# Kernel tuning notes

Measured on AMD Instinct MI355X. Metric: run time of the kernel, lower is better.

## Reference

```python
import jax, jax.numpy as jnp
import numpy as np

HEADS = 8
EPS = 1e-4

def pixel_norm(x):
    # faithful to source: mean over dim=1 (token axis for [B,T,C] tensors)
    return x / jnp.sqrt(jnp.mean(x * x, axis=1, keepdims=True) + EPS)

def setup_inputs() -> dict:
    key = jax.random.key(0)
    ks = jax.random.split(key, 6)
    B, T, C = 4, 2048, 512
    s = 1.0 / np.sqrt(C)
    return {
        "hidden_states": jax.random.normal(ks[0], (B, T, C), jnp.float32),
        "Wq": jax.random.normal(ks[1], (C, C), jnp.float32) * s,
        "Wk": jax.random.normal(ks[2], (C, C), jnp.float32) * s,
        "Wv": jax.random.normal(ks[3], (C, C), jnp.float32) * s,
        "Wo": jax.random.normal(ks[4], (C, C), jnp.float32) * s,
        "bo": jnp.zeros((C,), jnp.float32),
    }

def reference(hidden_states, Wq, Wk, Wv, Wo, bo):
    B, T, C = hidden_states.shape
    H = HEADS
    d = C // H
    scale = 1.0 / np.sqrt(d)  # attn.scale = head_dim**-0.5
    residual = hidden_states

    q = pixel_norm(hidden_states @ Wq)  # [B,T,C]
    k = pixel_norm(hidden_states @ Wk)
    v = pixel_norm(hidden_states @ Wv)

    # head_to_batch_dim: [B,T,C] -> [B,H,T,d]
    def split_heads(x):
        return x.reshape(B, T, H, d).transpose(0, 2, 1, 3)
    q, k, v = split_heads(q), split_heads(k), split_heads(v)

    scores = jnp.einsum("bhqd,bhkd->bhqk", q, k) * scale
    probs = jax.nn.softmax(scores, axis=-1)
    out = jnp.einsum("bhqk,bhkd->bhqd", probs, v)  # [B,H,T,d]

    # batch_to_head_dim: [B,H,T,d] -> [B,T,C]
    out = out.transpose(0, 2, 1, 3).reshape(B, T, C)
    out = out @ Wo + bo  # to_out[0]; to_out[1] is dropout (identity in eval)
    out = out + residual  # residual_connection
    return out  # rescale_output_factor = 1.0
```

## Files before the change

kernel.cpp:

```cpp
#include <hip/hip_runtime.h>

#define Tt 2048
#define Cc 512
#define Bb 4
#define BC (Bb * Cc)

typedef __attribute__((ext_vector_type(4))) float f32x4;
typedef __attribute__((ext_vector_type(8))) _Float16 f16x8;
typedef __attribute__((ext_vector_type(4))) _Float16 f16x4;
typedef __attribute__((ext_vector_type(2))) _Float16 f16x2;

__device__ static inline void gl16(const _Float16* g, _Float16* l)
{
    __builtin_amdgcn_global_load_lds(
        (const __attribute__((address_space(1))) void*)g,
        (__attribute__((address_space(3))) void*)l, 16, 0, 0);
}

__global__ __launch_bounds__(256) void prep(
    const float* __restrict__ Wq, const float* __restrict__ Wk,
    const float* __restrict__ Wv, const float* __restrict__ Wo,
    const float* __restrict__ HS, _Float16* __restrict__ Wt,
    _Float16* __restrict__ HSh, float* __restrict__ colsum)
{
    const int blk = blockIdx.x;
    const int tid = threadIdx.x;
    __shared__ float tile[64][65];

    if (blk < 2048) {
        const size_t i = ((size_t)blk * 256 + tid) * 8;
        float4 a = *(const float4*)&HS[i];
        float4 b = *(const float4*)&HS[i + 4];
        f16x8 o;
        o[0] = (_Float16)a.x; o[1] = (_Float16)a.y;
        o[2] = (_Float16)a.z; o[3] = (_Float16)a.w;
        o[4] = (_Float16)b.x; o[5] = (_Float16)b.y;
        o[6] = (_Float16)b.z; o[7] = (_Float16)b.w;
        *(f16x8*)&HSh[i] = o;
    } else if (blk < 2304) {
        const int lb = blk - 2048;
        const int z = lb >> 6, x = lb & 63;
        const float* W = (z == 0) ? Wq : (z == 1) ? Wk : (z == 2) ? Wv : Wo;
        const int k0 = (x >> 3) * 64, n0 = (x & 7) * 64;
#pragma unroll
        for (int i = 0; i < 4; ++i) {
            const int idx = i * 256 + tid;
            const int kr = idx >> 4, c4 = idx & 15;
            float4 v = *(const float4*)&W[(size_t)(k0 + kr) * Cc + n0 + c4 * 4];
            tile[kr][c4 * 4 + 0] = v.x; tile[kr][c4 * 4 + 1] = v.y;
            tile[kr][c4 * 4 + 2] = v.z; tile[kr][c4 * 4 + 3] = v.w;
        }
        __syncthreads();
#pragma unroll
        for (int i = 0; i < 4; ++i) {
            const int idx = i * 256 + tid;
            const int nr = idx >> 4, k4 = idx & 15;
            f16x4 o;
            o[0] = (_Float16)tile[k4 * 4 + 0][nr];
            o[1] = (_Float16)tile[k4 * 4 + 1][nr];
            o[2] = (_Float16)tile[k4 * 4 + 2][nr];
            o[3] = (_Float16)tile[k4 * 4 + 3][nr];
            *(f16x4*)&Wt[((size_t)(z * 512 + n0 + nr)) * Cc + k0 + k4 * 4] = o;
        }
    } else {
        const int i = (blk - 2304) * 2048 + tid * 8;
        *(f32x4*)&colsum[i]     = (f32x4){0.f, 0.f, 0.f, 0.f};
        *(f32x4*)&colsum[i + 4] = (f32x4){0.f, 0.f, 0.f, 0.f};
    }
}

__global__ __launch_bounds__(256, 3) void qkv_mfma(
    const _Float16* __restrict__ HSh, const _Float16* __restrict__ Wt,
    _Float16* __restrict__ Qf, _Float16* __restrict__ Kf,
    _Float16* __restrict__ Vf, float* __restrict__ colsum)
{
    const int mt = blockIdx.x;
    const int nt = blockIdx.y;
    const int z  = blockIdx.z;
    _Float16* Out = (z == 0) ? Qf : (z == 1) ? Kf : Vf;

    const int tid = threadIdx.x;
    const int wave = tid >> 6, lane = tid & 63;
    const int quad = lane >> 4, lm = lane & 15;
    const int wm = (wave & 1) * 64, wn = (wave >> 1) * 64;

    __shared__ _Float16 sA[128 * 32];
    __shared__ _Float16 sB[128 * 32];

    f32x4 acc[4][4];
#pragma unroll
    for (int mf = 0; mf < 4; ++mf)
#pragma unroll
        for (int nf = 0; nf < 4; ++nf) acc[mf][nf] = (f32x4){0.f, 0.f, 0.f, 0.f};

    const int lr = lane >> 2;
    const int lc = (lane & 3) * 8;
    const _Float16* gaA = HSh + (size_t)(mt * 128 + wave * 32 + lr) * Cc + lc;
    const _Float16* gaB = Wt + ((size_t)(z * 512 + nt * 128 + wave * 32 + lr)) * Cc + lc;
    _Float16* ldA = &sA[wave * 1024];
    _Float16* ldB = &sB[wave * 1024];

    for (int k0 = 0; k0 < Cc; k0 += 32) {
        __syncthreads();
        gl16(gaA + k0,            ldA);
        gl16(gaA + 16 * Cc + k0,  ldA + 512);
        gl16(gaB + k0,            ldB);
        gl16(gaB + 16 * Cc + k0,  ldB + 512);
        __syncthreads();

        f16x8 ah[4], bh[4];
#pragma unroll
        for (int mf = 0; mf < 4; ++mf)
            ah[mf] = *(const f16x8*)&sA[(wm + mf * 16 + lm) * 32 + quad * 8];
#pragma unroll
        for (int nf = 0; nf < 4; ++nf)
            bh[nf] = *(const f16x8*)&sB[(wn + nf * 16 + lm) * 32 + quad * 8];
#pragma unroll
        for (int mf = 0; mf < 4; ++mf)
#pragma unroll
            for (int nf = 0; nf < 4; ++nf)
                acc[mf][nf] = __builtin_amdgcn_mfma_f32_16x16x32_f16(ah[mf], bh[nf], acc[mf][nf], 0, 0, 0);
    }

    const int bidx = mt >> 4;
#pragma unroll
    for (int nf = 0; nf < 4; ++nf) {
        float cs = 0.f;
#pragma unroll
        for (int mf = 0; mf < 4; ++mf)
#pragma unroll
            for (int r = 0; r < 4; ++r) {
                const float v = acc[mf][nf][r];
                const size_t idx =
                    (size_t)(mt * 128 + wm + mf * 16 + quad * 4 + r) * Cc +
                    nt * 128 + wn + nf * 16 + lm;
                Out[idx] = (_Float16)v;
                cs += v * v;
            }
        cs += __shfl_xor(cs, 16, 64);
        cs += __shfl_xor(cs, 32, 64);
        if (lane < 16)
            atomicAdd(&colsum[(size_t)z * BC + bidx * Cc + nt * 128 + wn + nf * 16 + lane], cs);
    }
}

__global__ __launch_bounds__(256) void norm_vt(
    const _Float16* __restrict__ V, _Float16* __restrict__ VT,
    const float* __restrict__ colsum, float* __restrict__ inv)
{
    const int blk = blockIdx.x;
    const int tid = threadIdx.x;

    __shared__ _Float16 tile[64 * 72];

    if (blk >= 1024) {
        const int i = (blk - 1024) * 256 + tid;
        inv[i] = rsqrtf(colsum[i] * (1.0f / Tt) + 1e-4f);
        return;
    }

    const int b = blk >> 8, ct = (blk >> 5) & 7, tt = blk & 31;
    const int t0 = tt * 64, c0 = ct * 64;

#pragma unroll
    for (int i = 0; i < 2; ++i) {
        const int idx = i * 256 + tid;
        const int tr = idx >> 3, c8 = (idx & 7) * 8;
        *(f16x8*)&tile[tr * 72 + c8] =
            *(const f16x8*)&V[(size_t)(b * Tt + t0 + tr) * Cc + c0 + c8];
    }
    __syncthreads();
#pragma unroll
    for (int i = 0; i < 2; ++i) {
        const int idx = i * 256 + tid;
        const int cr = idx >> 3, u = idx & 7;
        const int C0 = ((u >> 2) & 1) * 32 + (u & 1) * 16 + ((u >> 1) & 1) * 4;
        f16x4 oa, ob;
#pragma unroll
        for (int j = 0; j < 4; ++j) oa[j] = tile[(u * 8 + j) * 72 + cr];
#pragma unroll
        for (int j = 0; j < 4; ++j) ob[j] = tile[(u * 8 + 4 + j) * 72 + cr];
        _Float16* dst = &VT[(size_t)(b * Cc + c0 + cr) * Tt + t0];
        *(f16x4*)&dst[C0]     = oa;
        *(f16x4*)&dst[C0 + 8] = ob;
    }
}

#define LSTR 72

__global__ __launch_bounds__(256, 2) void attn_mfma(
    const _Float16* __restrict__ Qf, const _Float16* __restrict__ Kf,
    const _Float16* __restrict__ VT, const float* __restrict__ inv,
    _Float16* __restrict__ AO)
{
    const int bid = blockIdx.x;
    const int qt = bid >> 5;
    const int bh = bid & 31;
    const int b = bh >> 3, h = bh & 7;
    const int tid = threadIdx.x;
    const int wave = tid >> 6, lane = tid & 63;
    const int quad = lane >> 4, lm = lane & 15;

    __shared__ _Float16 sK[2][64 * LSTR];
    __shared__ _Float16 sVT[2][2][64 * LSTR];

    f16x8 qb[2][2];
    {
        const float* iqp = inv + b * Cc + h * 64;
        const float* ikp = inv + BC + b * Cc + h * 64;
#pragma unroll
        for (int qf = 0; qf < 2; ++qf) {
            const int row = qt * 128 + wave * 32 + qf * 16 + lm;
#pragma unroll
            for (int ks = 0; ks < 2; ++ks) {
                const int d0 = ks * 32 + quad * 8;
                f16x8 qv = *(const f16x8*)&Qf[(size_t)(b * Tt + row) * Cc + h * 64 + d0];
#pragma unroll
                for (int j = 0; j < 8; ++j) {
                    const float f = (float)qv[j] * iqp[d0 + j] * ikp[d0 + j] * 0.18033688011f;
                    qb[qf][ks][j] = (_Float16)f;
                }
            }
        }
    }

    f32x4 o[4][2];
#pragma unroll
    for (int cf = 0; cf < 4; ++cf)
#pragma unroll
        for (int qf = 0; qf < 2; ++qf) o[cf][qf] = (f32x4){0.f, 0.f, 0.f, 0.f};
    f32x4 ol[2];
#pragma unroll
    for (int qf = 0; qf < 2; ++qf) ol[qf] = (f32x4){0.f, 0.f, 0.f, 0.f};
    f16x8 ones;
#pragma unroll
    for (int j = 0; j < 8; ++j) ones[j] = (_Float16)1.0f;

    f16x8 pb[2][2];
#pragma unroll
    for (int qf = 0; qf < 2; ++qf)
#pragma unroll
        for (int ks = 0; ks < 2; ++ks)
#pragma unroll
            for (int j = 0; j < 8; ++j) pb[qf][ks][j] = (_Float16)0.0f;

    const int sr0 = tid >> 3, sc0 = (tid & 7) * 8;
    const int sr1 = sr0 + 32;
    const _Float16* gK = Kf + (size_t)b * Tt * Cc + h * 64;
    const _Float16* gV = VT + ((size_t)b * Cc + h * 64) * Tt;

    f16x8 rka0, rka1, rva0, rva1;
    f16x8 rkb0, rkb1, rvb0, rvb1;
    {
        rka0 = *(const f16x8*)&gK[(size_t)sr0 * Cc + sc0];
        rka1 = *(const f16x8*)&gK[(size_t)sr1 * Cc + sc0];
        rva0 = *(const f16x8*)&gV[(size_t)sr0 * Tt + sc0];
        rva1 = *(const f16x8*)&gV[(size_t)sr1 * Tt + sc0];
        rkb0 = *(const f16x8*)&gK[(size_t)(64 + sr0) * Cc + sc0];
        rkb1 = *(const f16x8*)&gK[(size_t)(64 + sr1) * Cc + sc0];
        rvb0 = *(const f16x8*)&gV[(size_t)sr0 * Tt + 64 + sc0];
        rvb1 = *(const f16x8*)&gV[(size_t)sr1 * Tt + 64 + sc0];
    }

#pragma unroll 2
    for (int r = 0; r < 16; ++r) {
        const int g = r & 1;

        __syncthreads();
        *(f16x8*)&sK[0][sr0 * LSTR + sc0] = rka0;
        *(f16x8*)&sK[0][sr1 * LSTR + sc0] = rka1;
        *(f16x8*)&sVT[g][0][sr0 * LSTR + sc0] = rva0;
        *(f16x8*)&sVT[g][0][sr1 * LSTR + sc0] = rva1;
        *(f16x8*)&sK[1][sr0 * LSTR + sc0] = rkb0;
        *(f16x8*)&sK[1][sr1 * LSTR + sc0] = rkb1;
        *(f16x8*)&sVT[g][1][sr0 * LSTR + sc0] = rvb0;
        *(f16x8*)&sVT[g][1][sr1 * LSTR + sc0] = rvb1;
        __syncthreads();

        if (r < 15) {
            const int tn = (r + 1) * 128;
            rka0 = *(const f16x8*)&gK[(size_t)(tn + sr0) * Cc + sc0];
            rka1 = *(const f16x8*)&gK[(size_t)(tn + sr1) * Cc + sc0];
            rva0 = *(const f16x8*)&gV[(size_t)sr0 * Tt + tn + sc0];
            rva1 = *(const f16x8*)&gV[(size_t)sr1 * Tt + tn + sc0];
            rkb0 = *(const f16x8*)&gK[(size_t)(tn + 64 + sr0) * Cc + sc0];
            rkb1 = *(const f16x8*)&gK[(size_t)(tn + 64 + sr1) * Cc + sc0];
            rvb0 = *(const f16x8*)&gV[(size_t)sr0 * Tt + tn + 64 + sc0];
            rvb1 = *(const f16x8*)&gV[(size_t)sr1 * Tt + tn + 64 + sc0];
        }

#pragma unroll
        for (int half = 0; half < 2; ++half) {
            f32x4 st[4][2];
#pragma unroll
            for (int kf = 0; kf < 4; ++kf)
#pragma unroll
                for (int qf = 0; qf < 2; ++qf) st[kf][qf] = (f32x4){0.f, 0.f, 0.f, 0.f};
#pragma unroll
            for (int ks = 0; ks < 2; ++ks) {
                f16x8 ka[4];
#pragma unroll
                for (int kf = 0; kf < 4; ++kf)
                    ka[kf] = *(const f16x8*)&sK[half][(kf * 16 + lm) * LSTR + ks * 32 + quad * 8];
                __builtin_amdgcn_s_setprio(1);
#pragma unroll
                for (int kf = 0; kf < 4; ++kf)
#pragma unroll
                    for (int qf = 0; qf < 2; ++qf)
                        st[kf][qf] = __builtin_amdgcn_mfma_f32_16x16x32_f16(ka[kf], qb[qf][ks], st[kf][qf], 0, 0, 0);
                __builtin_amdgcn_s_setprio(0);
            }

            if (half == 1 || r > 0) {
                const _Float16* sVp = (half == 0) ? sVT[g ^ 1][1] : sVT[g][0];
#pragma unroll
                for (int ks = 0; ks < 2; ++ks) {
                    f16x8 va[4];
#pragma unroll
                    for (int cf = 0; cf < 4; ++cf)
                        va[cf] = *(const f16x8*)&sVp[(cf * 16 + lm) * LSTR + ks * 32 + quad * 8];
                    __builtin_amdgcn_s_setprio(1);
#pragma unroll
                    for (int cf = 0; cf < 4; ++cf)
#pragma unroll
                        for (int qf = 0; qf < 2; ++qf)
                            o[cf][qf] = __builtin_amdgcn_mfma_f32_16x16x32_f16(va[cf], pb[qf][ks], o[cf][qf], 0, 0, 0);
#pragma unroll
                    for (int qf = 0; qf < 2; ++qf)
                        ol[qf] = __builtin_amdgcn_mfma_f32_16x16x32_f16(ones, pb[qf][ks], ol[qf], 0, 0, 0);
                    __builtin_amdgcn_s_setprio(0);
                }
            }

#pragma unroll
            for (int ks = 0; ks < 2; ++ks)
#pragma unroll
                for (int qf = 0; qf < 2; ++qf) {
                    const f32x4 a = st[2 * ks][qf];
                    const f32x4 c = st[2 * ks + 1][qf];
                    const f16x2 l0 = __builtin_bit_cast(f16x2, __builtin_amdgcn_cvt_pkrtz(
                        __builtin_amdgcn_exp2f(a[0]), __builtin_amdgcn_exp2f(a[1])));
                    const f16x2 l1 = __builtin_bit_cast(f16x2, __builtin_amdgcn_cvt_pkrtz(
                        __builtin_amdgcn_exp2f(a[2]), __builtin_amdgcn_exp2f(a[3])));
                    const f16x2 h0 = __builtin_bit_cast(f16x2, __builtin_amdgcn_cvt_pkrtz(
                        __builtin_amdgcn_exp2f(c[0]), __builtin_amdgcn_exp2f(c[1])));
                    const f16x2 h1 = __builtin_bit_cast(f16x2, __builtin_amdgcn_cvt_pkrtz(
                        __builtin_amdgcn_exp2f(c[2]), __builtin_amdgcn_exp2f(c[3])));
                    f16x8 p;
                    p[0] = l0[0]; p[1] = l0[1]; p[2] = l1[0]; p[3] = l1[1];
                    p[4] = h0[0]; p[5] = h0[1]; p[6] = h1[0]; p[7] = h1[1];
                    pb[qf][ks] = p;
                }
        }
    }

    {
        const _Float16* sVp = sVT[1][1];
#pragma unroll
        for (int ks = 0; ks < 2; ++ks) {
            f16x8 va[4];
#pragma unroll
            for (int cf = 0; cf < 4; ++cf)
                va[cf] = *(const f16x8*)&sVp[(cf * 16 + lm) * LSTR + ks * 32 + quad * 8];
#pragma unroll
            for (int cf = 0; cf < 4; ++cf)
#pragma unroll
                for (int qf = 0; qf < 2; ++qf)
                    o[cf][qf] = __builtin_amdgcn_mfma_f32_16x16x32_f16(va[cf], pb[qf][ks], o[cf][qf], 0, 0, 0);
#pragma unroll
            for (int qf = 0; qf < 2; ++qf)
                ol[qf] = __builtin_amdgcn_mfma_f32_16x16x32_f16(ones, pb[qf][ks], ol[qf], 0, 0, 0);
        }
    }

    float il[2];
#pragma unroll
    for (int qf = 0; qf < 2; ++qf) il[qf] = 1.0f / ol[qf][0];
    const float* ivp = inv + 2 * BC + b * Cc + h * 64;
    float iv[4][4];
#pragma unroll
    for (int cf = 0; cf < 4; ++cf) {
        float4 t = *(const float4*)&ivp[cf * 16 + quad * 4];
        iv[cf][0] = t.x; iv[cf][1] = t.y; iv[cf][2] = t.z; iv[cf][3] = t.w;
    }
#pragma unroll
    for (int qf = 0; qf < 2; ++qf) {
        const size_t row = (size_t)(b * Tt + qt * 128 + wave * 32 + qf * 16 + lm);
#pragma unroll
        for (int cf = 0; cf < 4; ++cf) {
            f16x4 pk;
#pragma unroll
            for (int r = 0; r < 4; ++r)
                pk[r] = (_Float16)(o[cf][qf][r] * il[qf] * iv[cf][r]);
            *(f16x4*)&AO[row * Cc + h * 64 + cf * 16 + quad * 4] = pk;
        }
    }
}

__global__ __launch_bounds__(256, 2) void out_mfma(
    const _Float16* __restrict__ AO, const _Float16* __restrict__ Wt,
    const float* __restrict__ bo, const float* __restrict__ HS,
    float* __restrict__ Outp)
{
    const int mt = blockIdx.x;
    const int nt = blockIdx.y;
    const int tid = threadIdx.x;
    const int wave = tid >> 6, lane = tid & 63;
    const int quad = lane >> 4, lm = lane & 15;
    const int wm = (wave & 1) * 32, wn = (wave >> 1) * 64;

    __shared__ _Float16 sA[64 * 32];
    __shared__ _Float16 sB[128 * 32];

    f32x4 acc[2][4];
#pragma unroll
    for (int mf = 0; mf < 2; ++mf)
#pragma unroll
        for (int nf = 0; nf < 4; ++nf) acc[mf][nf] = (f32x4){0.f, 0.f, 0.f, 0.f};

    const int lr = lane >> 2;
    const int lc = (lane & 3) * 8;
    const _Float16* gaA = AO + (size_t)(mt * 64 + wave * 16 + lr) * Cc + lc;
    const _Float16* gaB = Wt + ((size_t)(3 * 512 + nt * 128 + wave * 32 + lr)) * Cc + lc;
    _Float16* ldA = &sA[wave * 512];
    _Float16* ldB = &sB[wave * 1024];

    for (int k0 = 0; k0 < Cc; k0 += 32) {
        __syncthreads();
        gl16(gaA + k0,           ldA);
        gl16(gaB + k0,           ldB);
        gl16(gaB + 16 * Cc + k0, ldB + 512);
        __syncthreads();

        f16x8 ah[2], bh[4];
#pragma unroll
        for (int mf = 0; mf < 2; ++mf)
            ah[mf] = *(const f16x8*)&sA[(wm + mf * 16 + lm) * 32 + quad * 8];
#pragma unroll
        for (int nf = 0; nf < 4; ++nf)
            bh[nf] = *(const f16x8*)&sB[(wn + nf * 16 + lm) * 32 + quad * 8];
#pragma unroll
        for (int mf = 0; mf < 2; ++mf)
#pragma unroll
            for (int nf = 0; nf < 4; ++nf)
                acc[mf][nf] = __builtin_amdgcn_mfma_f32_16x16x32_f16(ah[mf], bh[nf], acc[mf][nf], 0, 0, 0);
    }

#pragma unroll
    for (int mf = 0; mf < 2; ++mf)
#pragma unroll
        for (int r = 0; r < 4; ++r) {
            const size_t m = (size_t)(mt * 64 + wm + mf * 16 + quad * 4 + r);
#pragma unroll
            for (int nf = 0; nf < 4; ++nf) {
                const int col = nt * 128 + wn + nf * 16 + lm;
                Outp[m * Cc + col] = acc[mf][nf][r] + bo[col] + HS[m * Cc + col];
            }
        }
}

extern "C" void kernel_launch(void* const* d_in, const int* in_sizes, int n_in,
                              void* d_out, int out_size, void* d_ws,
                              size_t ws_size, hipStream_t stream)
{
    const float* HS = (const float*)d_in[0];
    const float* Wq = (const float*)d_in[1];
    const float* Wk = (const float*)d_in[2];
    const float* Wv = (const float*)d_in[3];
    const float* Wo = (const float*)d_in[4];
    const float* bo = (const float*)d_in[5];
    float* out = (float*)d_out;

    const size_t SZ = (size_t)Bb * Tt * Cc;
    _Float16* Qf  = (_Float16*)d_ws;
    _Float16* Kf  = Qf + SZ;
    _Float16* Vf  = Kf + SZ;
    _Float16* VTh = Vf + SZ;
    _Float16* AO  = VTh + SZ;
    _Float16* Wt  = AO + SZ;
    float* colsum = (float*)(Wt + 4 * Cc * Cc);
    float* inv    = colsum + 3 * BC;

    _Float16* HSh = VTh;

    prep<<<2307, 256, 0, stream>>>(Wq, Wk, Wv, Wo, HS, Wt, HSh, colsum);

    qkv_mfma<<<dim3(64, 4, 3), 256, 0, stream>>>(HSh, Wt, Qf, Kf, Vf, colsum);

    norm_vt<<<1048, 256, 0, stream>>>(Vf, VTh, colsum, inv);

    attn_mfma<<<dim3(512), 256, 0, stream>>>(Qf, Kf, VTh, inv, AO);

    out_mfma<<<dim3(128, 4), 256, 0, stream>>>(AO, Wt, bo, HS, out);
}
```

Baseline: 163.5 us.

## Use two waves per attention block with 64 query rows each

The attention kernel now launches 128 threads, two waves, instead of four, and each wave handles 64 query rows instead of 32. The K/V tile per iteration shrinks from 128 to 64 keys over 32 iterations, and shared memory for V drops to a simple double buffer. This doubles reuse of each LDS K/V fragment across query fragments and cuts LDS traffic per MFMA. In exchange it raises register pressure (o, st, qb and pb all double), uses launch bounds of 1, and halves the waves per block, which may reduce latency hiding.

```diff
diff --git a/kernel.cpp b/kernel.cpp
--- a/kernel.cpp
+++ b/kernel.cpp
@@ -188,7 +188,7 @@
 
 #define LSTR 72
 
-__global__ __launch_bounds__(256, 2) void attn_mfma(
+__global__ __launch_bounds__(128, 1) void attn_mfma(
     const _Float16* __restrict__ Qf, const _Float16* __restrict__ Kf,
     const _Float16* __restrict__ VT, const float* __restrict__ inv,
     _Float16* __restrict__ AO)
@@ -202,15 +202,15 @@
     const int quad = lane >> 4, lm = lane & 15;
 
     __shared__ _Float16 sK[2][64 * LSTR];
-    __shared__ _Float16 sVT[2][2][64 * LSTR];
-
-    f16x8 qb[2][2];
+    __shared__ _Float16 sVT[2][64 * LSTR];
+
+    f16x8 qb[4][2];
     {
         const float* iqp = inv + b * Cc + h * 64;
         const float* ikp = inv + BC + b * Cc + h * 64;
 #pragma unroll
-        for (int qf = 0; qf < 2; ++qf) {
-            const int row = qt * 128 + wave * 32 + qf * 16 + lm;
+        for (int qf = 0; qf < 4; ++qf) {
+            const int row = qt * 128 + wave * 64 + qf * 16 + lm;
 #pragma unroll
             for (int ks = 0; ks < 2; ++ks) {
                 const int d0 = ks * 32 + quad * 8;
@@ -224,138 +224,123 @@
         }
     }
 
-    f32x4 o[4][2];
+    f32x4 o[4][4];
 #pragma unroll
     for (int cf = 0; cf < 4; ++cf)
 #pragma unroll
-        for (int qf = 0; qf < 2; ++qf) o[cf][qf] = (f32x4){0.f, 0.f, 0.f, 0.f};
-    f32x4 ol[2];
-#pragma unroll
-    for (int qf = 0; qf < 2; ++qf) ol[qf] = (f32x4){0.f, 0.f, 0.f, 0.f};
+        for (int qf = 0; qf < 4; ++qf) o[cf][qf] = (f32x4){0.f, 0.f, 0.f, 0.f};
+    f32x4 ol[4];
+#pragma unroll
+    for (int qf = 0; qf < 4; ++qf) ol[qf] = (f32x4){0.f, 0.f, 0.f, 0.f};
     f16x8 ones;
 #pragma unroll
     for (int j = 0; j < 8; ++j) ones[j] = (_Float16)1.0f;
 
-    f16x8 pb[2][2];
-#pragma unroll
-    for (int qf = 0; qf < 2; ++qf)
+    f16x8 pb[4][2];
+#pragma unroll
+    for (int qf = 0; qf < 4; ++qf)
 #pragma unroll
         for (int ks = 0; ks < 2; ++ks)
 #pragma unroll
             for (int j = 0; j < 8; ++j) pb[qf][ks][j] = (_Float16)0.0f;
 
-    const int sr0 = tid >> 3, sc0 = (tid & 7) * 8;
-    const int sr1 = sr0 + 32;
+    const int sr = tid >> 3, sc = (tid & 7) * 8;
     const _Float16* gK = Kf + (size_t)b * Tt * Cc + h * 64;
     const _Float16* gV = VT + ((size_t)b * Cc + h * 64) * Tt;
 
-    f16x8 rka0, rka1, rva0, rva1;
-    f16x8 rkb0, rkb1, rvb0, rvb1;
+    f16x8 rk[4], rv[4];
+#pragma unroll
+    for (int i = 0; i < 4; ++i) {
+        rk[i] = *(const f16x8*)&gK[(size_t)(sr + i * 16) * Cc + sc];
+        rv[i] = *(const f16x8*)&gV[(size_t)(sr + i * 16) * Tt + sc];
+    }
+
+    for (int kt = 0; kt < 32; ++kt) {
+        const int cur = kt & 1, prv = cur ^ 1;
+        _Float16* sKc = sK[cur];
+        _Float16* sVc = sVT[cur];
+
+        __syncthreads();
+#pragma unroll
+        for (int i = 0; i < 4; ++i) {
+            *(f16x8*)&sKc[(sr + i * 16) * LSTR + sc] = rk[i];
+            *(f16x8*)&sVc[(sr + i * 16) * LSTR + sc] = rv[i];
+        }
+        __syncthreads();
+
+        if (kt < 31) {
+            const int t0 = (kt + 1) * 64;
+#pragma unroll
+            for (int i = 0; i < 4; ++i) {
+                rk[i] = *(const f16x8*)&gK[(size_t)(t0 + sr + i * 16) * Cc + sc];
+                rv[i] = *(const f16x8*)&gV[(size_t)(sr + i * 16) * Tt + t0 + sc];
+            }
+        }
+
+        f32x4 st[4][4];
+#pragma unroll
+        for (int kf = 0; kf < 4; ++kf)
+#pragma unroll
+            for (int qf = 0; qf < 4; ++qf) st[kf][qf] = (f32x4){0.f, 0.f, 0.f, 0.f};
+#pragma unroll
+        for (int ks = 0; ks < 2; ++ks) {
+            f16x8 ka[4];
+#pragma unroll
+            for (int kf = 0; kf < 4; ++kf)
+                ka[kf] = *(const f16x8*)&sKc[(kf * 16 + lm) * LSTR + ks * 32 + quad * 8];
+            __builtin_amdgcn_s_setprio(1);
+#pragma unroll
+            for (int kf = 0; kf < 4; ++kf)
+#pragma unroll
+                for (int qf = 0; qf < 4; ++qf)
+                    st[kf][qf] = __builtin_amdgcn_mfma_f32_16x16x32_f16(ka[kf], qb[qf][ks], st[kf][qf], 0, 0, 0);
+            __builtin_amdgcn_s_setprio(0);
+        }
+
+        if (kt > 0) {
+            _Float16* sVp = sVT[prv];
+#pragma unroll
+            for (int ks = 0; ks < 2; ++ks) {
+                f16x8 va[4];
+#pragma unroll
+                for (int cf = 0; cf < 4; ++cf)
+                    va[cf] = *(const f16x8*)&sVp[(cf * 16 + lm) * LSTR + ks * 32 + quad * 8];
+                __builtin_amdgcn_s_setprio(1);
+#pragma unroll
+                for (int cf = 0; cf < 4; ++cf)
+#pragma unroll
+                    for (int qf = 0; qf < 4; ++qf)
+                        o[cf][qf] = __builtin_amdgcn_mfma_f32_16x16x32_f16(va[cf], pb[qf][ks], o[cf][qf], 0, 0, 0);
+#pragma unroll
+                for (int qf = 0; qf < 4; ++qf)
+                    ol[qf] = __builtin_amdgcn_mfma_f32_16x16x32_f16(ones, pb[qf][ks], ol[qf], 0, 0, 0);
+                __builtin_amdgcn_s_setprio(0);
+            }
+        }
+
+#pragma unroll
+        for (int ks = 0; ks < 2; ++ks)
+#pragma unroll
+            for (int qf = 0; qf < 4; ++qf) {
+                const f32x4 a = st[2 * ks][qf];
+                const f32x4 c = st[2 * ks + 1][qf];
+                const f16x2 l0 = __builtin_bit_cast(f16x2, __builtin_amdgcn_cvt_pkrtz(
+                    __builtin_amdgcn_exp2f(a[0]), __builtin_amdgcn_exp2f(a[1])));
+                const f16x2 l1 = __builtin_bit_cast(f16x2, __builtin_amdgcn_cvt_pkrtz(
+                    __builtin_amdgcn_exp2f(a[2]), __builtin_amdgcn_exp2f(a[3])));
+                const f16x2 h0 = __builtin_bit_cast(f16x2, __builtin_amdgcn_cvt_pkrtz(
+                    __builtin_amdgcn_exp2f(c[0]), __builtin_amdgcn_exp2f(c[1])));
+                const f16x2 h1 = __builtin_bit_cast(f16x2, __builtin_amdgcn_cvt_pkrtz(
+                    __builtin_amdgcn_exp2f(c[2]), __builtin_amdgcn_exp2f(c[3])));
+                f16x8 p;
+                p[0] = l0[0]; p[1] = l0[1]; p[2] = l1[0]; p[3] = l1[1];
+                p[4] = h0[0]; p[5] = h0[1]; p[6] = h1[0]; p[7] = h1[1];
+                pb[qf][ks] = p;
+            }
+    }
+
     {
-        rka0 = *(const f16x8*)&gK[(size_t)sr0 * Cc + sc0];
-        rka1 = *(const f16x8*)&gK[(size_t)sr1 * Cc + sc0];
-        rva0 = *(const f16x8*)&gV[(size_t)sr0 * Tt + sc0];
-        rva1 = *(const f16x8*)&gV[(size_t)sr1 * Tt + sc0];
-        rkb0 = *(const f16x8*)&gK[(size_t)(64 + sr0) * Cc + sc0];
-        rkb1 = *(const f16x8*)&gK[(size_t)(64 + sr1) * Cc + sc0];
-        rvb0 = *(const f16x8*)&gV[(size_t)sr0 * Tt + 64 + sc0];
-        rvb1 = *(const f16x8*)&gV[(size_t)sr1 * Tt + 64 + sc0];
-    }
-
-#pragma unroll 2
-    for (int r = 0; r < 16; ++r) {
-        const int g = r & 1;
-
-        __syncthreads();
-        *(f16x8*)&sK[0][sr0 * LSTR + sc0] = rka0;
-        *(f16x8*)&sK[0][sr1 * LSTR + sc0] = rka1;
-        *(f16x8*)&sVT[g][0][sr0 * LSTR + sc0] = rva0;
-        *(f16x8*)&sVT[g][0][sr1 * LSTR + sc0] = rva1;
-        *(f16x8*)&sK[1][sr0 * LSTR + sc0] = rkb0;
-        *(f16x8*)&sK[1][sr1 * LSTR + sc0] = rkb1;
-        *(f16x8*)&sVT[g][1][sr0 * LSTR + sc0] = rvb0;
-        *(f16x8*)&sVT[g][1][sr1 * LSTR + sc0] = rvb1;
-        __syncthreads();
-
-        if (r < 15) {
-            const int tn = (r + 1) * 128;
-            rka0 = *(const f16x8*)&gK[(size_t)(tn + sr0) * Cc + sc0];
-            rka1 = *(const f16x8*)&gK[(size_t)(tn + sr1) * Cc + sc0];
-            rva0 = *(const f16x8*)&gV[(size_t)sr0 * Tt + tn + sc0];
-            rva1 = *(const f16x8*)&gV[(size_t)sr1 * Tt + tn + sc0];
-            rkb0 = *(const f16x8*)&gK[(size_t)(tn + 64 + sr0) * Cc + sc0];
-            rkb1 = *(const f16x8*)&gK[(size_t)(tn + 64 + sr1) * Cc + sc0];
-            rvb0 = *(const f16x8*)&gV[(size_t)sr0 * Tt + tn + 64 + sc0];
-            rvb1 = *(const f16x8*)&gV[(size_t)sr1 * Tt + tn + 64 + sc0];
-        }
-
-#pragma unroll
-        for (int half = 0; half < 2; ++half) {
-            f32x4 st[4][2];
-#pragma unroll
-            for (int kf = 0; kf < 4; ++kf)
-#pragma unroll
-                for (int qf = 0; qf < 2; ++qf) st[kf][qf] = (f32x4){0.f, 0.f, 0.f, 0.f};
-#pragma unroll
-            for (int ks = 0; ks < 2; ++ks) {
-                f16x8 ka[4];
-#pragma unroll
-                for (int kf = 0; kf < 4; ++kf)
-                    ka[kf] = *(const f16x8*)&sK[half][(kf * 16 + lm) * LSTR + ks * 32 + quad * 8];
-                __builtin_amdgcn_s_setprio(1);
-#pragma unroll
-                for (int kf = 0; kf < 4; ++kf)
-#pragma unroll
-                    for (int qf = 0; qf < 2; ++qf)
-                        st[kf][qf] = __builtin_amdgcn_mfma_f32_16x16x32_f16(ka[kf], qb[qf][ks], st[kf][qf], 0, 0, 0);
-                __builtin_amdgcn_s_setprio(0);
-            }
-
-            if (half == 1 || r > 0) {
-                const _Float16* sVp = (half == 0) ? sVT[g ^ 1][1] : sVT[g][0];
-#pragma unroll
-                for (int ks = 0; ks < 2; ++ks) {
-                    f16x8 va[4];
-#pragma unroll
-                    for (int cf = 0; cf < 4; ++cf)
-                        va[cf] = *(const f16x8*)&sVp[(cf * 16 + lm) * LSTR + ks * 32 + quad * 8];
-                    __builtin_amdgcn_s_setprio(1);
-#pragma unroll
-                    for (int cf = 0; cf < 4; ++cf)
-#pragma unroll
-                        for (int qf = 0; qf < 2; ++qf)
-                            o[cf][qf] = __builtin_amdgcn_mfma_f32_16x16x32_f16(va[cf], pb[qf][ks], o[cf][qf], 0, 0, 0);
-#pragma unroll
-                    for (int qf = 0; qf < 2; ++qf)
-                        ol[qf] = __builtin_amdgcn_mfma_f32_16x16x32_f16(ones, pb[qf][ks], ol[qf], 0, 0, 0);
-                    __builtin_amdgcn_s_setprio(0);
-                }
-            }
-
-#pragma unroll
-            for (int ks = 0; ks < 2; ++ks)
-#pragma unroll
-                for (int qf = 0; qf < 2; ++qf) {
-                    const f32x4 a = st[2 * ks][qf];
-                    const f32x4 c = st[2 * ks + 1][qf];
-                    const f16x2 l0 = __builtin_bit_cast(f16x2, __builtin_amdgcn_cvt_pkrtz(
-                        __builtin_amdgcn_exp2f(a[0]), __builtin_amdgcn_exp2f(a[1])));
-                    const f16x2 l1 = __builtin_bit_cast(f16x2, __builtin_amdgcn_cvt_pkrtz(
-                        __builtin_amdgcn_exp2f(a[2]), __builtin_amdgcn_exp2f(a[3])));
-                    const f16x2 h0 = __builtin_bit_cast(f16x2, __builtin_amdgcn_cvt_pkrtz(
-                        __builtin_amdgcn_exp2f(c[0]), __builtin_amdgcn_exp2f(c[1])));
-                    const f16x2 h1 = __builtin_bit_cast(f16x2, __builtin_amdgcn_cvt_pkrtz(
-                        __builtin_amdgcn_exp2f(c[2]), __builtin_amdgcn_exp2f(c[3])));
-                    f16x8 p;
-                    p[0] = l0[0]; p[1] = l0[1]; p[2] = l1[0]; p[3] = l1[1];
-                    p[4] = h0[0]; p[5] = h0[1]; p[6] = h1[0]; p[7] = h1[1];
-                    pb[qf][ks] = p;
-                }
-        }
-    }
-
-    {
-        const _Float16* sVp = sVT[1][1];
+        _Float16* sVp = sVT[1];
 #pragma unroll
         for (int ks = 0; ks < 2; ++ks) {
             f16x8 va[4];
@@ -365,17 +350,17 @@
 #pragma unroll
             for (int cf = 0; cf < 4; ++cf)
 #pragma unroll
-                for (int qf = 0; qf < 2; ++qf)
+                for (int qf = 0; qf < 4; ++qf)
                     o[cf][qf] = __builtin_amdgcn_mfma_f32_16x16x32_f16(va[cf], pb[qf][ks], o[cf][qf], 0, 0, 0);
 #pragma unroll
-            for (int qf = 0; qf < 2; ++qf)
+            for (int qf = 0; qf < 4; ++qf)
                 ol[qf] = __builtin_amdgcn_mfma_f32_16x16x32_f16(ones, pb[qf][ks], ol[qf], 0, 0, 0);
         }
     }
 
-    float il[2];
-#pragma unroll
-    for (int qf = 0; qf < 2; ++qf) il[qf] = 1.0f / ol[qf][0];
+    float il[4];
+#pragma unroll
+    for (int qf = 0; qf < 4; ++qf) il[qf] = 1.0f / ol[qf][0];
     const float* ivp = inv + 2 * BC + b * Cc + h * 64;
     float iv[4][4];
 #pragma unroll
@@ -384,8 +369,8 @@
         iv[cf][0] = t.x; iv[cf][1] = t.y; iv[cf][2] = t.z; iv[cf][3] = t.w;
     }
 #pragma unroll
-    for (int qf = 0; qf < 2; ++qf) {
-        const size_t row = (size_t)(b * Tt + qt * 128 + wave * 32 + qf * 16 + lm);
+    for (int qf = 0; qf < 4; ++qf) {
+        const size_t row = (size_t)(b * Tt + qt * 128 + wave * 64 + qf * 16 + lm);
 #pragma unroll
         for (int cf = 0; cf < 4; ++cf) {
             f16x4 pk;
@@ -489,7 +474,7 @@
 
     norm_vt<<<1048, 256, 0, stream>>>(Vf, VTh, colsum, inv);
 
-    attn_mfma<<<dim3(512), 256, 0, stream>>>(Qf, Kf, VTh, inv, AO);
+    attn_mfma<<<dim3(512), 128, 0, stream>>>(Qf, Kf, VTh, inv, AO);
 
     out_mfma<<<dim3(128, 4), 256, 0, stream>>>(AO, Wt, bo, HS, out);
 }
```

Result: slower. 173.7 us (+6.2%).
